# Performance work log

Hardware: AMD Instinct MI355X
Metric: run time of the kernel (lower is better)

Reference implementation:

```python
import jax, jax.numpy as jnp
import numpy as np

INPUT_DIM, HIDDEN, NUM_CLASSES = 16, 128, 24
B, T = 4096, 1024  # raw I/Q frame (B, 2, T); seq_len = 2*T/INPUT_DIM = 128


def setup_inputs() -> dict:
    key = jax.random.key(0)
    ks = jax.random.split(key, 12)
    s = 1.0 / np.sqrt(HIDDEN)  # torch default uniform bound ~ use scaled normal
    def w(k, shape, scale):
        return jax.random.normal(k, shape, jnp.float32) * scale
    return {
        "x": jax.random.normal(ks[0], (B, 2, T), jnp.float32),
        "w_ih1": w(ks[1], (3 * HIDDEN, INPUT_DIM), s),
        "w_hh1": w(ks[2], (3 * HIDDEN, HIDDEN), s),
        "b_ih1": w(ks[3], (3 * HIDDEN,), s),
        "b_hh1": w(ks[4], (3 * HIDDEN,), s),
        "w_ih2": w(ks[5], (3 * HIDDEN, HIDDEN), s),
        "w_hh2": w(ks[6], (3 * HIDDEN, HIDDEN), s),
        "b_ih2": w(ks[7], (3 * HIDDEN,), s),
        "b_hh2": w(ks[8], (3 * HIDDEN,), s),
        "fc_w": w(ks[9], (NUM_CLASSES, HIDDEN), s),
        "fc_b": w(ks[10], (NUM_CLASSES,), s),
    }


def _gru_layer(x, w_ih, w_hh, b_ih, b_hh, return_seq=True):
    # x: (B, L, D). PyTorch GRU gate order: r, z, n.
    Bb = x.shape[0]
    H = w_hh.shape[1]
    xp = jnp.einsum('bld,gd->blg', x, w_ih) + b_ih  # (B, L, 3H) precomputed input proj

    def step(h, xt):
        gh = h @ w_hh.T + b_hh  # (B, 3H)
        ir, iz, inn = jnp.split(xt, 3, axis=-1)
        hr, hz, hn = jnp.split(gh, 3, axis=-1)
        r = jax.nn.sigmoid(ir + hr)
        z = jax.nn.sigmoid(iz + hz)
        n = jnp.tanh(inn + r * hn)
        h_new = (1.0 - z) * n + z * h
        return h_new, (h_new if return_seq else 0.0)

    h0 = jnp.zeros((Bb, H), x.dtype)
    h_last, ys = jax.lax.scan(step, h0, jnp.swapaxes(xp, 0, 1))
    if return_seq:
        return jnp.swapaxes(ys, 0, 1)
    return h_last


def reference(x, w_ih1, w_hh1, b_ih1, b_hh1, w_ih2, w_hh2, b_ih2, b_hh2, fc_w, fc_b):
    Bb = x.shape[0]
    # (B,2,T) -> (B,2,L,8) -> (B,L,2,8) -> (B,L,16)
    h = x.reshape(Bb, 2, -1, INPUT_DIM // 2)
    h = jnp.swapaxes(h, 1, 2).reshape(Bb, -1, INPUT_DIM)
    seq1 = _gru_layer(h, w_ih1, w_hh1, b_ih1, b_hh1, return_seq=True)
    last = _gru_layer(seq1, w_ih2, w_hh2, b_ih2, b_hh2, return_seq=False)
    return last @ fc_w.T + fc_b
```

## Files before the change

### kernel.cpp

```cpp
#include <hip/hip_runtime.h>


typedef _Float16 half_t;
typedef _Float16 half8 __attribute__((ext_vector_type(8)));
typedef _Float16 half4v __attribute__((ext_vector_type(4)));
typedef float f32x4 __attribute__((ext_vector_type(4)));

#define BB 16
#define HS 136
#define XS 520

static __device__ __forceinline__ f32x4 mfma16(half8 a, half8 b, f32x4 c) {
  return __builtin_amdgcn_mfma_f32_16x16x32_f16(a, b, c, 0, 0, 0);
}

static __device__ __forceinline__ void pin(half8& v) {
  f32x4 t = __builtin_bit_cast(f32x4, v);
  asm volatile("" : "+v"(t));
  v = __builtin_bit_cast(half8, t);
}

static __device__ __forceinline__ half8 zero8() {
  half8 v;
#pragma unroll
  for (int i = 0; i < 8; ++i) v[i] = (half_t)0.f;
  return v;
}

static __device__ __forceinline__ half8 ldw8(const float* __restrict__ p) {
  float4 a = *(const float4*)p;
  float4 b = *(const float4*)(p + 4);
  half8 r;
  r[0] = (half_t)a.x; r[1] = (half_t)a.y; r[2] = (half_t)a.z; r[3] = (half_t)a.w;
  r[4] = (half_t)b.x; r[5] = (half_t)b.y; r[6] = (half_t)b.z; r[7] = (half_t)b.w;
  return r;
}

static __device__ __forceinline__ float sigm(float v) {
  return __builtin_amdgcn_rcpf(1.f + __expf(-v));
}
static __device__ __forceinline__ float tanh_fast(float v) {
  float e = __expf(2.f * v);
  return 1.f - 2.f * __builtin_amdgcn_rcpf(1.f + e);
}

__global__ __launch_bounds__(512, 2) void gru_fused(
    const float* __restrict__ x,
    const float* __restrict__ wih1, const float* __restrict__ whh1,
    const float* __restrict__ bih1, const float* __restrict__ bhh1,
    const float* __restrict__ wih2, const float* __restrict__ whh2,
    const float* __restrict__ bih2, const float* __restrict__ bhh2,
    const float* __restrict__ fcw, const float* __restrict__ fcb,
    float* __restrict__ out)
{
  __shared__ __align__(16) half_t xl[BB][XS];
  __shared__ __align__(16) half_t h1b[2][BB][HS];
  __shared__ __align__(16) half_t h2b[2][BB][HS];
  __shared__ float h2f[BB][129];

  const int tid = threadIdx.x;
  const int lane = tid & 63;
  const int wv = tid >> 6;
  const int q = lane >> 4;
  const int c = lane & 15;
  const int jc = wv * 16 + c;
  const int s0 = blockIdx.x * BB;

  for (int i = tid; i < 2 * BB * HS; i += 512) {
    ((half_t*)h1b)[i] = (half_t)0.f;
    ((half_t*)h2b)[i] = (half_t)0.f;
  }

  const float b1r  = bih1[jc]       + bhh1[jc];
  const float b1z  = bih1[128 + jc] + bhh1[128 + jc];
  const float b1in = bih1[256 + jc];
  const float b1hn = bhh1[256 + jc];
  const float b2r  = bih2[jc]       + bhh2[jc];
  const float b2z  = bih2[128 + jc] + bhh2[128 + jc];
  const float b2in = bih2[256 + jc];
  const float b2hn = bhh2[256 + jc];

  half8 wi1r, wi1z, wi1n;
  if (q < 2) {
    wi1r = ldw8(wih1 + (0 * 128 + jc) * 16 + q * 8);
    wi1z = ldw8(wih1 + (1 * 128 + jc) * 16 + q * 8);
    wi1n = ldw8(wih1 + (2 * 128 + jc) * 16 + q * 8);
  } else {
    wi1r = zero8(); wi1z = zero8(); wi1n = zero8();
  }
  pin(wi1r); pin(wi1z); pin(wi1n);

  half8 wh1r[4], wh1z[4], wh1n[4], wi2r[4], wi2z[4], wi2n[4], wh2r[4], wh2z[4], wh2n[4];
#pragma unroll
  for (int kk = 0; kk < 4; ++kk) {
    const int ko = kk * 32 + q * 8;
    wh1r[kk] = ldw8(whh1 + (0 * 128 + jc) * 128 + ko);
    wh1z[kk] = ldw8(whh1 + (1 * 128 + jc) * 128 + ko);
    wh1n[kk] = ldw8(whh1 + (2 * 128 + jc) * 128 + ko);
    wi2r[kk] = ldw8(wih2 + (0 * 128 + jc) * 128 + ko);
    wi2z[kk] = ldw8(wih2 + (1 * 128 + jc) * 128 + ko);
    wi2n[kk] = ldw8(wih2 + (2 * 128 + jc) * 128 + ko);
    wh2r[kk] = ldw8(whh2 + (0 * 128 + jc) * 128 + ko);
    wh2z[kk] = ldw8(whh2 + (1 * 128 + jc) * 128 + ko);
    wh2n[kk] = ldw8(whh2 + (2 * 128 + jc) * 128 + ko);
    pin(wh1r[kk]); pin(wh1z[kk]); pin(wh1n[kk]);
    pin(wi2r[kk]); pin(wi2z[kk]); pin(wi2n[kk]);
    pin(wh2r[kk]); pin(wh2z[kk]); pin(wh2n[kk]);
  }

  float h1p[4] = {0.f, 0.f, 0.f, 0.f};
  float h2p[4] = {0.f, 0.f, 0.f, 0.f};

  for (int tc = 0; tc < 4; ++tc) {
#pragma unroll
    for (int it = 0; it < 4; ++it) {
      int idx = tid + it * 512;
      int s = idx >> 7;
      int rem = idx & 127;
      int ch = rem >> 6;
      int i4 = rem & 63;
      const float4 v = *(const float4*)(x + (size_t)(s0 + s) * 2048 + ch * 1024 + tc * 256 + i4 * 4);
      half4v hv;
      hv[0] = (half_t)v.x; hv[1] = (half_t)v.y; hv[2] = (half_t)v.z; hv[3] = (half_t)v.w;
      *(half4v*)&xl[s][(i4 >> 1) * 16 + ch * 8 + (i4 & 1) * 4] = hv;
    }
    __syncthreads();

    for (int tt = 0; tt < 32; ++tt) {
      const int i = tc * 32 + tt;
      const int rb = i & 1;
      const int wb = rb ^ 1;

      f32x4 ar  = {b1r, b1r, b1r, b1r};
      f32x4 az  = {b1z, b1z, b1z, b1z};
      f32x4 ain = {b1in, b1in, b1in, b1in};
      f32x4 ahn = {b1hn, b1hn, b1hn, b1hn};
      f32x4 cr  = {b2r, b2r, b2r, b2r};
      f32x4 cz  = {b2z, b2z, b2z, b2z};
      f32x4 cin = {b2in, b2in, b2in, b2in};
      f32x4 chn = {b2hn, b2hn, b2hn, b2hn};

      {
        half8 ax = zero8();
        if (q < 2) ax = *(const half8*)&xl[c][tt * 16 + q * 8];
        ar  = mfma16(ax, wi1r, ar);
        az  = mfma16(ax, wi1z, az);
        ain = mfma16(ax, wi1n, ain);
      }
#pragma unroll
      for (int kk = 0; kk < 4; ++kk) {
        half8 ah = *(const half8*)&h1b[rb][c][kk * 32 + q * 8];
        half8 a2 = *(const half8*)&h2b[rb][c][kk * 32 + q * 8];
        ar  = mfma16(ah, wh1r[kk], ar);
        az  = mfma16(ah, wh1z[kk], az);
        ahn = mfma16(ah, wh1n[kk], ahn);
        cr  = mfma16(ah, wi2r[kk], cr);
        cz  = mfma16(ah, wi2z[kk], cz);
        cin = mfma16(ah, wi2n[kk], cin);
        cr  = mfma16(a2, wh2r[kk], cr);
        cz  = mfma16(a2, wh2z[kk], cz);
        chn = mfma16(a2, wh2n[kk], chn);
      }

#pragma unroll
      for (int r = 0; r < 4; ++r) {
        float rg = sigm(ar[r]);
        float zg = sigm(az[r]);
        float ng = tanh_fast(fmaf(rg, ahn[r], ain[r]));
        float hn = fmaf(zg, h1p[r] - ng, ng);
        h1p[r] = hn;
        h1b[wb][q * 4 + r][jc] = (half_t)hn;
      }
      if (i > 0) {
#pragma unroll
        for (int r = 0; r < 4; ++r) {
          float rg = sigm(cr[r]);
          float zg = sigm(cz[r]);
          float ng = tanh_fast(fmaf(rg, chn[r], cin[r]));
          float hn = fmaf(zg, h2p[r] - ng, ng);
          h2p[r] = hn;
          h2b[wb][q * 4 + r][jc] = (half_t)hn;
        }
      }
      __syncthreads();
    }
  }

  {
    f32x4 cr  = {b2r, b2r, b2r, b2r};
    f32x4 cz  = {b2z, b2z, b2z, b2z};
    f32x4 cin = {b2in, b2in, b2in, b2in};
    f32x4 chn = {b2hn, b2hn, b2hn, b2hn};
#pragma unroll
    for (int kk = 0; kk < 4; ++kk) {
      half8 a1 = *(const half8*)&h1b[0][c][kk * 32 + q * 8];
      half8 a2 = *(const half8*)&h2b[0][c][kk * 32 + q * 8];
      cr  = mfma16(a1, wi2r[kk], cr);
      cz  = mfma16(a1, wi2z[kk], cz);
      cin = mfma16(a1, wi2n[kk], cin);
      cr  = mfma16(a2, wh2r[kk], cr);
      cz  = mfma16(a2, wh2z[kk], cz);
      chn = mfma16(a2, wh2n[kk], chn);
    }
#pragma unroll
    for (int r = 0; r < 4; ++r) {
      float rg = sigm(cr[r]);
      float zg = sigm(cz[r]);
      float ng = tanh_fast(fmaf(rg, chn[r], cin[r]));
      h2p[r] = fmaf(zg, h2p[r] - ng, ng);
    }
  }

#pragma unroll
  for (int r = 0; r < 4; ++r) h2f[q * 4 + r][jc] = h2p[r];
  __syncthreads();
  if (tid < 384) {
    const int m = tid & 15;
    const int cls = tid >> 4;
    const float* w = fcw + cls * 128;
    float acc = fcb[cls];
#pragma unroll 8
    for (int j = 0; j < 128; ++j) acc = fmaf(h2f[m][j], w[j], acc);
    out[(size_t)(s0 + m) * 24 + cls] = acc;
  }
}

extern "C" void kernel_launch(void* const* d_in, const int* in_sizes, int n_in,
                              void* d_out, int out_size, void* d_ws, size_t ws_size,
                              hipStream_t stream) {
  (void)in_sizes; (void)n_in; (void)d_ws; (void)ws_size; (void)out_size;
  const float* x    = (const float*)d_in[0];
  const float* wih1 = (const float*)d_in[1];
  const float* whh1 = (const float*)d_in[2];
  const float* bih1 = (const float*)d_in[3];
  const float* bhh1 = (const float*)d_in[4];
  const float* wih2 = (const float*)d_in[5];
  const float* whh2 = (const float*)d_in[6];
  const float* bih2 = (const float*)d_in[7];
  const float* bhh2 = (const float*)d_in[8];
  const float* fcw  = (const float*)d_in[9];
  const float* fcb  = (const float*)d_in[10];
  float* outp = (float*)d_out;
  gru_fused<<<dim3(256), dim3(512), 0, stream>>>(
      x, wih1, whh1, bih1, bhh1, wih2, whh2, bih2, bhh2, fcw, fcb, outp);
}
```

Before: 277.3 us.

## Split fused two-layer GRU into separate layer kernels via fp16 workspace sequence

Replaces the single fused wavefront-style kernel with two kernels when the workspace is large enough. Layer 1 writes its hidden sequence in fp16 to global workspace in 8-step chunks, and layer 2 reads it back with register prefetch and double buffering. The aim is to cut per-kernel register pressure and shorten the per-step critical path. In exchange it adds about 128 MB of global write plus read traffic and serialises the two layers instead of overlapping them. The asm pin helpers are also removed.

```diff
diff --git a/kernel.cpp b/kernel.cpp
--- a/kernel.cpp
+++ b/kernel.cpp
@@ -12,12 +12,6 @@
 
 static __device__ __forceinline__ f32x4 mfma16(half8 a, half8 b, f32x4 c) {
   return __builtin_amdgcn_mfma_f32_16x16x32_f16(a, b, c, 0, 0, 0);
-}
-
-static __device__ __forceinline__ void pin(half8& v) {
-  f32x4 t = __builtin_bit_cast(f32x4, v);
-  asm volatile("" : "+v"(t));
-  v = __builtin_bit_cast(half8, t);
 }
 
 static __device__ __forceinline__ half8 zero8() {
@@ -42,6 +36,238 @@
 static __device__ __forceinline__ float tanh_fast(float v) {
   float e = __expf(2.f * v);
   return 1.f - 2.f * __builtin_amdgcn_rcpf(1.f + e);
+}
+
+__global__ __launch_bounds__(512, 2) void gru_l1(
+    const float* __restrict__ x,
+    const float* __restrict__ wih1, const float* __restrict__ whh1,
+    const float* __restrict__ bih1, const float* __restrict__ bhh1,
+    half_t* __restrict__ seq1)
+{
+  __shared__ __align__(16) half_t xl[BB][XS];
+  __shared__ __align__(16) half_t ost[8][BB][HS];
+
+  const int tid = threadIdx.x;
+  const int lane = tid & 63;
+  const int wv = tid >> 6;
+  const int q = lane >> 4;
+  const int c = lane & 15;
+  const int jc = wv * 16 + c;
+  const int s0 = blockIdx.x * BB;
+
+  for (int i = tid; i < 8 * BB * HS; i += 512) ((half_t*)ost)[i] = (half_t)0.f;
+
+  const float b1r  = bih1[jc]       + bhh1[jc];
+  const float b1z  = bih1[128 + jc] + bhh1[128 + jc];
+  const float b1in = bih1[256 + jc];
+  const float b1hn = bhh1[256 + jc];
+
+  half8 wi1r, wi1z, wi1n;
+  if (q < 2) {
+    wi1r = ldw8(wih1 + (0 * 128 + jc) * 16 + q * 8);
+    wi1z = ldw8(wih1 + (1 * 128 + jc) * 16 + q * 8);
+    wi1n = ldw8(wih1 + (2 * 128 + jc) * 16 + q * 8);
+  } else {
+    wi1r = zero8(); wi1z = zero8(); wi1n = zero8();
+  }
+  half8 wh1r[4], wh1z[4], wh1n[4];
+#pragma unroll
+  for (int kk = 0; kk < 4; ++kk) {
+    const int ko = kk * 32 + q * 8;
+    wh1r[kk] = ldw8(whh1 + (0 * 128 + jc) * 128 + ko);
+    wh1z[kk] = ldw8(whh1 + (1 * 128 + jc) * 128 + ko);
+    wh1n[kk] = ldw8(whh1 + (2 * 128 + jc) * 128 + ko);
+  }
+
+  float h1p[4] = {0.f, 0.f, 0.f, 0.f};
+
+  for (int g = 0; g < 16; ++g) {
+    if ((g & 3) == 0) {
+      const int tc = g >> 2;
+#pragma unroll
+      for (int it = 0; it < 4; ++it) {
+        int idx = tid + it * 512;
+        int s = idx >> 7;
+        int rem = idx & 127;
+        int ch = rem >> 6;
+        int i4 = rem & 63;
+        const float4 v = *(const float4*)(x + (size_t)(s0 + s) * 2048 + ch * 1024 + tc * 256 + i4 * 4);
+        half4v hv;
+        hv[0] = (half_t)v.x; hv[1] = (half_t)v.y; hv[2] = (half_t)v.z; hv[3] = (half_t)v.w;
+        *(half4v*)&xl[s][(i4 >> 1) * 16 + ch * 8 + (i4 & 1) * 4] = hv;
+      }
+      __syncthreads();
+    }
+
+    for (int tt = 0; tt < 8; ++tt) {
+      const int i = g * 8 + tt;
+      const int prev = (i + 7) & 7;
+
+      f32x4 ar  = {b1r, b1r, b1r, b1r};
+      f32x4 az  = {b1z, b1z, b1z, b1z};
+      f32x4 ain = {b1in, b1in, b1in, b1in};
+      f32x4 ahn = {b1hn, b1hn, b1hn, b1hn};
+      {
+        half8 ax = zero8();
+        if (q < 2) ax = *(const half8*)&xl[c][(i & 31) * 16 + q * 8];
+        ar  = mfma16(ax, wi1r, ar);
+        az  = mfma16(ax, wi1z, az);
+        ain = mfma16(ax, wi1n, ain);
+      }
+#pragma unroll
+      for (int kk = 0; kk < 4; ++kk) {
+        half8 ah = *(const half8*)&ost[prev][c][kk * 32 + q * 8];
+        ar  = mfma16(ah, wh1r[kk], ar);
+        az  = mfma16(ah, wh1z[kk], az);
+        ahn = mfma16(ah, wh1n[kk], ahn);
+      }
+#pragma unroll
+      for (int r = 0; r < 4; ++r) {
+        float rg = sigm(ar[r]);
+        float zg = sigm(az[r]);
+        float ng = tanh_fast(fmaf(rg, ahn[r], ain[r]));
+        float hn = fmaf(zg, h1p[r] - ng, ng);
+        h1p[r] = hn;
+        ost[tt][q * 4 + r][jc] = (half_t)hn;
+      }
+      __syncthreads();
+    }
+
+#pragma unroll
+    for (int p = 0; p < 4; ++p) {
+      int idx = tid + p * 512;
+      int col16 = idx & 15;
+      int row = (idx >> 4) & 15;
+      int st = idx >> 8;
+      f32x4 v = *(const f32x4*)&ost[st][row][col16 * 8];
+      size_t off = ((size_t)((s0 + row) * 128 + (g * 8 + st))) * 128 + col16 * 8;
+      *(f32x4*)(seq1 + off) = v;
+    }
+    __syncthreads();
+  }
+}
+
+__global__ __launch_bounds__(512, 2) void gru_l2(
+    const half_t* __restrict__ seq1,
+    const float* __restrict__ wih2, const float* __restrict__ whh2,
+    const float* __restrict__ bih2, const float* __restrict__ bhh2,
+    const float* __restrict__ fcw, const float* __restrict__ fcb,
+    float* __restrict__ out)
+{
+  __shared__ __align__(16) half_t sc[2][8][BB][HS];
+  __shared__ __align__(16) half_t h2b[2][BB][HS];
+  __shared__ float h2f[BB][129];
+
+  const int tid = threadIdx.x;
+  const int lane = tid & 63;
+  const int wv = tid >> 6;
+  const int q = lane >> 4;
+  const int c = lane & 15;
+  const int jc = wv * 16 + c;
+  const int s0 = blockIdx.x * BB;
+
+  for (int i = tid; i < BB * HS; i += 512) ((half_t*)h2b[0])[i] = (half_t)0.f;
+
+  const float b2r  = bih2[jc]       + bhh2[jc];
+  const float b2z  = bih2[128 + jc] + bhh2[128 + jc];
+  const float b2in = bih2[256 + jc];
+  const float b2hn = bhh2[256 + jc];
+
+  half8 wi2r[4], wi2z[4], wi2n[4], wh2r[4], wh2z[4], wh2n[4];
+#pragma unroll
+  for (int kk = 0; kk < 4; ++kk) {
+    const int ko = kk * 32 + q * 8;
+    wi2r[kk] = ldw8(wih2 + (0 * 128 + jc) * 128 + ko);
+    wi2z[kk] = ldw8(wih2 + (1 * 128 + jc) * 128 + ko);
+    wi2n[kk] = ldw8(wih2 + (2 * 128 + jc) * 128 + ko);
+    wh2r[kk] = ldw8(whh2 + (0 * 128 + jc) * 128 + ko);
+    wh2z[kk] = ldw8(whh2 + (1 * 128 + jc) * 128 + ko);
+    wh2n[kk] = ldw8(whh2 + (2 * 128 + jc) * 128 + ko);
+  }
+
+#pragma unroll
+  for (int p = 0; p < 4; ++p) {
+    int idx = tid + p * 512;
+    int col16 = idx & 15;
+    int row = (idx >> 4) & 15;
+    int st = idx >> 8;
+    size_t off = ((size_t)((s0 + row) * 128 + st)) * 128 + col16 * 8;
+    *(f32x4*)&sc[0][st][row][col16 * 8] = *(const f32x4*)(seq1 + off);
+  }
+  __syncthreads();
+
+  float h2p[4] = {0.f, 0.f, 0.f, 0.f};
+
+  for (int ch = 0; ch < 16; ++ch) {
+    f32x4 pf[4];
+    if (ch < 15) {
+#pragma unroll
+      for (int p = 0; p < 4; ++p) {
+        int idx = tid + p * 512;
+        int col16 = idx & 15;
+        int row = (idx >> 4) & 15;
+        int st = idx >> 8;
+        size_t off = ((size_t)((s0 + row) * 128 + ((ch + 1) * 8 + st))) * 128 + col16 * 8;
+        pf[p] = *(const f32x4*)(seq1 + off);
+      }
+    }
+    const int cb = ch & 1;
+
+    for (int tt = 0; tt < 8; ++tt) {
+      const int i = ch * 8 + tt;
+      const int rb = i & 1;
+      const int wb = rb ^ 1;
+
+      f32x4 cr  = {b2r, b2r, b2r, b2r};
+      f32x4 cz  = {b2z, b2z, b2z, b2z};
+      f32x4 cin = {b2in, b2in, b2in, b2in};
+      f32x4 chn = {b2hn, b2hn, b2hn, b2hn};
+#pragma unroll
+      for (int kk = 0; kk < 4; ++kk) {
+        half8 a1 = *(const half8*)&sc[cb][tt][c][kk * 32 + q * 8];
+        half8 a2 = *(const half8*)&h2b[rb][c][kk * 32 + q * 8];
+        cr  = mfma16(a1, wi2r[kk], cr);
+        cz  = mfma16(a1, wi2z[kk], cz);
+        cin = mfma16(a1, wi2n[kk], cin);
+        cr  = mfma16(a2, wh2r[kk], cr);
+        cz  = mfma16(a2, wh2z[kk], cz);
+        chn = mfma16(a2, wh2n[kk], chn);
+      }
+#pragma unroll
+      for (int r = 0; r < 4; ++r) {
+        float rg = sigm(cr[r]);
+        float zg = sigm(cz[r]);
+        float ng = tanh_fast(fmaf(rg, chn[r], cin[r]));
+        float hn = fmaf(zg, h2p[r] - ng, ng);
+        h2p[r] = hn;
+        h2b[wb][q * 4 + r][jc] = (half_t)hn;
+      }
+      if (tt == 7 && ch < 15) {
+#pragma unroll
+        for (int p = 0; p < 4; ++p) {
+          int idx = tid + p * 512;
+          int col16 = idx & 15;
+          int row = (idx >> 4) & 15;
+          int st = idx >> 8;
+          *(f32x4*)&sc[cb ^ 1][st][row][col16 * 8] = pf[p];
+        }
+      }
+      __syncthreads();
+    }
+  }
+
+#pragma unroll
+  for (int r = 0; r < 4; ++r) h2f[q * 4 + r][jc] = h2p[r];
+  __syncthreads();
+  if (tid < 384) {
+    const int m = tid & 15;
+    const int cls = tid >> 4;
+    const float* w = fcw + cls * 128;
+    float acc = fcb[cls];
+#pragma unroll 8
+    for (int j = 0; j < 128; ++j) acc = fmaf(h2f[m][j], w[j], acc);
+    out[(size_t)(s0 + m) * 24 + cls] = acc;
+  }
 }
 
 __global__ __launch_bounds__(512, 2) void gru_fused(
@@ -88,8 +314,6 @@
   } else {
     wi1r = zero8(); wi1z = zero8(); wi1n = zero8();
   }
-  pin(wi1r); pin(wi1z); pin(wi1n);
-
   half8 wh1r[4], wh1z[4], wh1n[4], wi2r[4], wi2z[4], wi2n[4], wh2r[4], wh2z[4], wh2n[4];
 #pragma unroll
   for (int kk = 0; kk < 4; ++kk) {
@@ -103,9 +327,6 @@
     wh2r[kk] = ldw8(whh2 + (0 * 128 + jc) * 128 + ko);
     wh2z[kk] = ldw8(whh2 + (1 * 128 + jc) * 128 + ko);
     wh2n[kk] = ldw8(whh2 + (2 * 128 + jc) * 128 + ko);
-    pin(wh1r[kk]); pin(wh1z[kk]); pin(wh1n[kk]);
-    pin(wi2r[kk]); pin(wi2z[kk]); pin(wi2n[kk]);
-    pin(wh2r[kk]); pin(wh2z[kk]); pin(wh2n[kk]);
   }
 
   float h1p[4] = {0.f, 0.f, 0.f, 0.f};
@@ -228,7 +449,7 @@
 extern "C" void kernel_launch(void* const* d_in, const int* in_sizes, int n_in,
                               void* d_out, int out_size, void* d_ws, size_t ws_size,
                               hipStream_t stream) {
-  (void)in_sizes; (void)n_in; (void)d_ws; (void)ws_size; (void)out_size;
+  (void)in_sizes; (void)n_in; (void)out_size;
   const float* x    = (const float*)d_in[0];
   const float* wih1 = (const float*)d_in[1];
   const float* whh1 = (const float*)d_in[2];
@@ -241,6 +462,14 @@
   const float* fcw  = (const float*)d_in[9];
   const float* fcb  = (const float*)d_in[10];
   float* outp = (float*)d_out;
-  gru_fused<<<dim3(256), dim3(512), 0, stream>>>(
-      x, wih1, whh1, bih1, bhh1, wih2, whh2, bih2, bhh2, fcw, fcb, outp);
-}
+
+  const size_t seq_bytes = (size_t)4096 * 128 * 128 * sizeof(half_t);
+  if (ws_size >= seq_bytes) {
+    half_t* seq1 = (half_t*)d_ws;
+    gru_l1<<<dim3(256), dim3(512), 0, stream>>>(x, wih1, whh1, bih1, bhh1, seq1);
+    gru_l2<<<dim3(256), dim3(512), 0, stream>>>(seq1, wih2, whh2, bih2, bhh2, fcw, fcb, outp);
+  } else {
+    gru_fused<<<dim3(256), dim3(512), 0, stream>>>(
+        x, wih1, whh1, bih1, bhh1, wih2, whh2, bih2, bhh2, fcw, fcb, outp);
+  }
+}
```

Measured after the change: 295.9 us. 6.7% more time.

## Split fused GRU into per-layer kernels with producer/consumer warp specialization

Applied to the files above, without the earlier changes.

Replaces the single fused two-layer kernel with two kernels: layer 1 writes its fp16 hidden sequence to workspace, and layer 2 reads it back and applies the final linear layer. Each kernel uses 1024 threads. Eight producer waves compute the input projection one step ahead into double-buffered LDS, while eight consumer waves run only the recurrent matmul and gates. The recurrence critical path per step drops from nine MFMAs per k-slice to three. The cost is a round trip of about 128 MB of intermediate sequence through global memory, and the whole path depends on the workspace being large enough; otherwise it falls back to the fused kernel.

```diff
diff --git a/kernel.cpp b/kernel.cpp
--- a/kernel.cpp
+++ b/kernel.cpp
@@ -6,18 +6,11 @@
 typedef _Float16 half4v __attribute__((ext_vector_type(4)));
 typedef float f32x4 __attribute__((ext_vector_type(4)));
 
-#define BB 16
 #define HS 136
 #define XS 520
 
 static __device__ __forceinline__ f32x4 mfma16(half8 a, half8 b, f32x4 c) {
   return __builtin_amdgcn_mfma_f32_16x16x32_f16(a, b, c, 0, 0, 0);
-}
-
-static __device__ __forceinline__ void pin(half8& v) {
-  f32x4 t = __builtin_bit_cast(f32x4, v);
-  asm volatile("" : "+v"(t));
-  v = __builtin_bit_cast(half8, t);
 }
 
 static __device__ __forceinline__ half8 zero8() {
@@ -42,6 +35,258 @@
 static __device__ __forceinline__ float tanh_fast(float v) {
   float e = __expf(2.f * v);
   return 1.f - 2.f * __builtin_amdgcn_rcpf(1.f + e);
+}
+
+__global__ __launch_bounds__(1024, 4) void gru_l1(
+    const float* __restrict__ x,
+    const float* __restrict__ wih1, const float* __restrict__ whh1,
+    const float* __restrict__ bih1, const float* __restrict__ bhh1,
+    half_t* __restrict__ seq1)
+{
+  __shared__ __align__(16) half_t xl[2][16][XS];
+  __shared__ __align__(16) half_t ost[8][16][HS];
+  __shared__ __align__(16) f32x4 xpb[2][8][3][64];
+
+  const int tid = threadIdx.x;
+  const int lane = tid & 63;
+  const int wv = tid >> 6;
+  const int q = lane >> 4;
+  const int c = lane & 15;
+  const bool prod = (wv >= 8);
+  const int cw = prod ? (wv - 8) : wv;
+  const int jc = cw * 16 + c;
+  const int s0 = blockIdx.x * 16;
+
+  for (int i = tid; i < 8 * 16 * HS; i += 1024) ((half_t*)ost)[i] = (half_t)0.f;
+
+#pragma unroll
+  for (int p = 0; p < 2; ++p) {
+    int idx = tid + p * 1024;
+    int s = idx >> 7, rem = idx & 127, chn = rem >> 6, i4 = rem & 63;
+    const float4 v = *(const float4*)(x + (size_t)(s0 + s) * 2048 + chn * 1024 + i4 * 4);
+    half4v hv;
+    hv[0] = (half_t)v.x; hv[1] = (half_t)v.y; hv[2] = (half_t)v.z; hv[3] = (half_t)v.w;
+    *(half4v*)&xl[0][s][(i4 >> 1) * 16 + chn * 8 + (i4 & 1) * 4] = hv;
+  }
+
+  half8 w[3][4];
+  if (prod) {
+#pragma unroll
+    for (int g = 0; g < 3; ++g) {
+      if (q < 2) w[g][0] = ldw8(wih1 + (g * 128 + jc) * 16 + q * 8);
+      else       w[g][0] = zero8();
+    }
+  } else {
+#pragma unroll
+    for (int g = 0; g < 3; ++g)
+#pragma unroll
+      for (int kk = 0; kk < 4; ++kk)
+        w[g][kk] = ldw8(whh1 + (g * 128 + jc) * 128 + kk * 32 + q * 8);
+  }
+  const float* bb = prod ? bih1 : bhh1;
+  const float b0 = bb[jc], b1 = bb[128 + jc], b2 = bb[256 + jc];
+
+  float h1p[4] = {0.f, 0.f, 0.f, 0.f};
+  __syncthreads();
+
+  if (prod) {
+    half8 ax = zero8();
+    if (q < 2) ax = *(const half8*)&xl[0][c][0 * 16 + q * 8];
+    f32x4 ir = {b0, b0, b0, b0}, iz = {b1, b1, b1, b1}, in_ = {b2, b2, b2, b2};
+    ir  = mfma16(ax, w[0][0], ir);
+    iz  = mfma16(ax, w[1][0], iz);
+    in_ = mfma16(ax, w[2][0], in_);
+    xpb[0][cw][0][lane] = ir; xpb[0][cw][1][lane] = iz; xpb[0][cw][2][lane] = in_;
+  }
+  __syncthreads();
+
+  for (int i = 0; i < 128; ++i) {
+    if ((i & 7) == 0 && i > 0) {
+      const int g8 = (i >> 3) - 1;
+#pragma unroll
+      for (int p = 0; p < 2; ++p) {
+        int idx = tid + p * 1024;
+        int col16 = idx & 15, row = (idx >> 4) & 15, st = idx >> 8;
+        f32x4 v = *(const f32x4*)&ost[st][row][col16 * 8];
+        *(f32x4*)(seq1 + ((size_t)((s0 + row) * 128 + g8 * 8 + st)) * 128 + col16 * 8) = v;
+      }
+      __syncthreads();
+    }
+
+    if (!prod) {
+      const int rd = (i + 7) & 7;
+      half8 f0 = *(const half8*)&ost[rd][c][0 * 32 + q * 8];
+      half8 f1 = *(const half8*)&ost[rd][c][1 * 32 + q * 8];
+      half8 f2 = *(const half8*)&ost[rd][c][2 * 32 + q * 8];
+      half8 f3 = *(const half8*)&ost[rd][c][3 * 32 + q * 8];
+      f32x4 xr = xpb[i & 1][cw][0][lane];
+      f32x4 xz = xpb[i & 1][cw][1][lane];
+      f32x4 xn = xpb[i & 1][cw][2][lane];
+      f32x4 hr = {b0, b0, b0, b0}, hz = {b1, b1, b1, b1}, hn = {b2, b2, b2, b2};
+      hr = mfma16(f0, w[0][0], hr); hz = mfma16(f0, w[1][0], hz); hn = mfma16(f0, w[2][0], hn);
+      hr = mfma16(f1, w[0][1], hr); hz = mfma16(f1, w[1][1], hz); hn = mfma16(f1, w[2][1], hn);
+      hr = mfma16(f2, w[0][2], hr); hz = mfma16(f2, w[1][2], hz); hn = mfma16(f2, w[2][2], hn);
+      hr = mfma16(f3, w[0][3], hr); hz = mfma16(f3, w[1][3], hz); hn = mfma16(f3, w[2][3], hn);
+#pragma unroll
+      for (int r = 0; r < 4; ++r) {
+        float rg = sigm(xr[r] + hr[r]);
+        float zg = sigm(xz[r] + hz[r]);
+        float ng = tanh_fast(fmaf(rg, hn[r], xn[r]));
+        float hne = fmaf(zg, h1p[r] - ng, ng);
+        h1p[r] = hne;
+        ost[i & 7][q * 4 + r][jc] = (half_t)hne;
+      }
+    } else {
+      if ((i & 7) == 0) {
+        int nc = (i >> 5) + 1;
+        if (nc < 4) {
+          int p = (i >> 3) & 3;
+          int idx = (wv - 8) * 64 + lane + p * 512;
+          int s = idx >> 7, rem = idx & 127, chn = rem >> 6, i4 = rem & 63;
+          const float4 v = *(const float4*)(x + (size_t)(s0 + s) * 2048 + chn * 1024 + nc * 256 + i4 * 4);
+          half4v hv;
+          hv[0] = (half_t)v.x; hv[1] = (half_t)v.y; hv[2] = (half_t)v.z; hv[3] = (half_t)v.w;
+          *(half4v*)&xl[nc & 1][s][(i4 >> 1) * 16 + chn * 8 + (i4 & 1) * 4] = hv;
+        }
+      }
+      if (i < 127) {
+        const int t1 = i + 1;
+        half8 ax = zero8();
+        if (q < 2) ax = *(const half8*)&xl[(t1 >> 5) & 1][c][(t1 & 31) * 16 + q * 8];
+        f32x4 ir = {b0, b0, b0, b0}, iz = {b1, b1, b1, b1}, in_ = {b2, b2, b2, b2};
+        ir  = mfma16(ax, w[0][0], ir);
+        iz  = mfma16(ax, w[1][0], iz);
+        in_ = mfma16(ax, w[2][0], in_);
+        xpb[t1 & 1][cw][0][lane] = ir;
+        xpb[t1 & 1][cw][1][lane] = iz;
+        xpb[t1 & 1][cw][2][lane] = in_;
+      }
+    }
+    __syncthreads();
+  }
+
+#pragma unroll
+  for (int p = 0; p < 2; ++p) {
+    int idx = tid + p * 1024;
+    int col16 = idx & 15, row = (idx >> 4) & 15, st = idx >> 8;
+    f32x4 v = *(const f32x4*)&ost[st][row][col16 * 8];
+    *(f32x4*)(seq1 + ((size_t)((s0 + row) * 128 + 15 * 8 + st)) * 128 + col16 * 8) = v;
+  }
+}
+
+__global__ __launch_bounds__(1024, 4) void gru_l2(
+    const half_t* __restrict__ seq1,
+    const float* __restrict__ wih2, const float* __restrict__ whh2,
+    const float* __restrict__ bih2, const float* __restrict__ bhh2,
+    const float* __restrict__ fcw, const float* __restrict__ fcb,
+    float* __restrict__ out)
+{
+  __shared__ __align__(16) half_t h2b[2][16][HS];
+  __shared__ __align__(16) f32x4 xpb[2][8][3][64];
+  __shared__ float h2f[16][132];
+
+  const int tid = threadIdx.x;
+  const int lane = tid & 63;
+  const int wv = tid >> 6;
+  const int q = lane >> 4;
+  const int c = lane & 15;
+  const bool prod = (wv >= 8);
+  const int cw = prod ? (wv - 8) : wv;
+  const int jc = cw * 16 + c;
+  const int s0 = blockIdx.x * 16;
+
+  for (int i = tid; i < 2 * 16 * HS; i += 1024) ((half_t*)h2b)[i] = (half_t)0.f;
+
+  const float* wbase = prod ? wih2 : whh2;
+  half8 w[3][4];
+#pragma unroll
+  for (int g = 0; g < 3; ++g)
+#pragma unroll
+    for (int kk = 0; kk < 4; ++kk)
+      w[g][kk] = ldw8(wbase + (g * 128 + jc) * 128 + kk * 32 + q * 8);
+  const float* bb = prod ? bih2 : bhh2;
+  const float b0 = bb[jc], b1 = bb[128 + jc], b2 = bb[256 + jc];
+
+  float h2p[4] = {0.f, 0.f, 0.f, 0.f};
+  f32x4 buf[2][4];
+
+  if (prod) {
+#pragma unroll
+    for (int kk = 0; kk < 4; ++kk)
+      buf[0][kk] = *(const f32x4*)(seq1 + ((size_t)(s0 + c) * 128 + 0) * 128 + kk * 32 + q * 8);
+    f32x4 ir = {b0, b0, b0, b0}, iz = {b1, b1, b1, b1}, in_ = {b2, b2, b2, b2};
+#pragma unroll
+    for (int kk = 0; kk < 4; ++kk) {
+      half8 a = __builtin_bit_cast(half8, buf[0][kk]);
+      ir  = mfma16(a, w[0][kk], ir);
+      iz  = mfma16(a, w[1][kk], iz);
+      in_ = mfma16(a, w[2][kk], in_);
+    }
+    xpb[0][cw][0][lane] = ir; xpb[0][cw][1][lane] = iz; xpb[0][cw][2][lane] = in_;
+#pragma unroll
+    for (int kk = 0; kk < 4; ++kk)
+      buf[1][kk] = *(const f32x4*)(seq1 + ((size_t)(s0 + c) * 128 + 1) * 128 + kk * 32 + q * 8);
+  }
+  __syncthreads();
+
+  for (int i = 0; i < 128; ++i) {
+    if (!prod) {
+      const int rs = (i + 1) & 1;
+      half8 f0 = *(const half8*)&h2b[rs][c][0 * 32 + q * 8];
+      half8 f1 = *(const half8*)&h2b[rs][c][1 * 32 + q * 8];
+      half8 f2 = *(const half8*)&h2b[rs][c][2 * 32 + q * 8];
+      half8 f3 = *(const half8*)&h2b[rs][c][3 * 32 + q * 8];
+      f32x4 xr = xpb[i & 1][cw][0][lane];
+      f32x4 xz = xpb[i & 1][cw][1][lane];
+      f32x4 xn = xpb[i & 1][cw][2][lane];
+      f32x4 hr = {b0, b0, b0, b0}, hz = {b1, b1, b1, b1}, hn = {b2, b2, b2, b2};
+      hr = mfma16(f0, w[0][0], hr); hz = mfma16(f0, w[1][0], hz); hn = mfma16(f0, w[2][0], hn);
+      hr = mfma16(f1, w[0][1], hr); hz = mfma16(f1, w[1][1], hz); hn = mfma16(f1, w[2][1], hn);
+      hr = mfma16(f2, w[0][2], hr); hz = mfma16(f2, w[1][2], hz); hn = mfma16(f2, w[2][2], hn);
+      hr = mfma16(f3, w[0][3], hr); hz = mfma16(f3, w[1][3], hz); hn = mfma16(f3, w[2][3], hn);
+#pragma unroll
+      for (int r = 0; r < 4; ++r) {
+        float rg = sigm(xr[r] + hr[r]);
+        float zg = sigm(xz[r] + hz[r]);
+        float ng = tanh_fast(fmaf(rg, hn[r], xn[r]));
+        float hne = fmaf(zg, h2p[r] - ng, ng);
+        h2p[r] = hne;
+        h2b[i & 1][q * 4 + r][jc] = (half_t)hne;
+      }
+    } else if (i < 127) {
+      const int bi = (i + 1) & 1;
+      if (i + 2 < 128) {
+#pragma unroll
+        for (int kk = 0; kk < 4; ++kk)
+          buf[bi ^ 1][kk] = *(const f32x4*)(seq1 + ((size_t)(s0 + c) * 128 + (i + 2)) * 128 + kk * 32 + q * 8);
+      }
+      f32x4 ir = {b0, b0, b0, b0}, iz = {b1, b1, b1, b1}, in_ = {b2, b2, b2, b2};
+#pragma unroll
+      for (int kk = 0; kk < 4; ++kk) {
+        half8 a = __builtin_bit_cast(half8, buf[bi][kk]);
+        ir  = mfma16(a, w[0][kk], ir);
+        iz  = mfma16(a, w[1][kk], iz);
+        in_ = mfma16(a, w[2][kk], in_);
+      }
+      xpb[bi][cw][0][lane] = ir; xpb[bi][cw][1][lane] = iz; xpb[bi][cw][2][lane] = in_;
+    }
+    __syncthreads();
+  }
+
+  if (!prod) {
+#pragma unroll
+    for (int r = 0; r < 4; ++r) h2f[q * 4 + r][jc] = h2p[r];
+  }
+  __syncthreads();
+  if (tid < 384) {
+    const int m = tid & 15;
+    const int cls = tid >> 4;
+    const float* fw = fcw + cls * 128;
+    float acc = fcb[cls];
+#pragma unroll 8
+    for (int j = 0; j < 128; ++j) acc = fmaf(h2f[m][j], fw[j], acc);
+    out[(size_t)(s0 + m) * 24 + cls] = acc;
+  }
 }
 
 __global__ __launch_bounds__(512, 2) void gru_fused(
@@ -53,10 +298,10 @@
     const float* __restrict__ fcw, const float* __restrict__ fcb,
     float* __restrict__ out)
 {
-  __shared__ __align__(16) half_t xl[BB][XS];
-  __shared__ __align__(16) half_t h1b[2][BB][HS];
-  __shared__ __align__(16) half_t h2b[2][BB][HS];
-  __shared__ float h2f[BB][129];
+  __shared__ __align__(16) half_t xl[16][XS];
+  __shared__ __align__(16) half_t h1b[2][16][HS];
+  __shared__ __align__(16) half_t h2b[2][16][HS];
+  __shared__ float h2f[16][129];
 
   const int tid = threadIdx.x;
   const int lane = tid & 63;
@@ -64,9 +309,9 @@
   const int q = lane >> 4;
   const int c = lane & 15;
   const int jc = wv * 16 + c;
-  const int s0 = blockIdx.x * BB;
-
-  for (int i = tid; i < 2 * BB * HS; i += 512) {
+  const int s0 = blockIdx.x * 16;
+
+  for (int i = tid; i < 2 * 16 * HS; i += 512) {
     ((half_t*)h1b)[i] = (half_t)0.f;
     ((half_t*)h2b)[i] = (half_t)0.f;
   }
@@ -88,8 +333,6 @@
   } else {
     wi1r = zero8(); wi1z = zero8(); wi1n = zero8();
   }
-  pin(wi1r); pin(wi1z); pin(wi1n);
-
   half8 wh1r[4], wh1z[4], wh1n[4], wi2r[4], wi2z[4], wi2n[4], wh2r[4], wh2z[4], wh2n[4];
 #pragma unroll
   for (int kk = 0; kk < 4; ++kk) {
@@ -103,9 +346,6 @@
     wh2r[kk] = ldw8(whh2 + (0 * 128 + jc) * 128 + ko);
     wh2z[kk] = ldw8(whh2 + (1 * 128 + jc) * 128 + ko);
     wh2n[kk] = ldw8(whh2 + (2 * 128 + jc) * 128 + ko);
-    pin(wh1r[kk]); pin(wh1z[kk]); pin(wh1n[kk]);
-    pin(wi2r[kk]); pin(wi2z[kk]); pin(wi2n[kk]);
-    pin(wh2r[kk]); pin(wh2z[kk]); pin(wh2n[kk]);
   }
 
   float h1p[4] = {0.f, 0.f, 0.f, 0.f};
@@ -117,12 +357,12 @@
       int idx = tid + it * 512;
       int s = idx >> 7;
       int rem = idx & 127;
-      int ch = rem >> 6;
+      int chn = rem >> 6;
       int i4 = rem & 63;
-      const float4 v = *(const float4*)(x + (size_t)(s0 + s) * 2048 + ch * 1024 + tc * 256 + i4 * 4);
+      const float4 v = *(const float4*)(x + (size_t)(s0 + s) * 2048 + chn * 1024 + tc * 256 + i4 * 4);
       half4v hv;
       hv[0] = (half_t)v.x; hv[1] = (half_t)v.y; hv[2] = (half_t)v.z; hv[3] = (half_t)v.w;
-      *(half4v*)&xl[s][(i4 >> 1) * 16 + ch * 8 + (i4 & 1) * 4] = hv;
+      *(half4v*)&xl[s][(i4 >> 1) * 16 + chn * 8 + (i4 & 1) * 4] = hv;
     }
     __syncthreads();
 
@@ -217,10 +457,10 @@
   if (tid < 384) {
     const int m = tid & 15;
     const int cls = tid >> 4;
-    const float* w = fcw + cls * 128;
+    const float* fw = fcw + cls * 128;
     float acc = fcb[cls];
 #pragma unroll 8
-    for (int j = 0; j < 128; ++j) acc = fmaf(h2f[m][j], w[j], acc);
+    for (int j = 0; j < 128; ++j) acc = fmaf(h2f[m][j], fw[j], acc);
     out[(size_t)(s0 + m) * 24 + cls] = acc;
   }
 }
@@ -228,7 +468,7 @@
 extern "C" void kernel_launch(void* const* d_in, const int* in_sizes, int n_in,
                               void* d_out, int out_size, void* d_ws, size_t ws_size,
                               hipStream_t stream) {
-  (void)in_sizes; (void)n_in; (void)d_ws; (void)ws_size; (void)out_size;
+  (void)in_sizes; (void)n_in; (void)out_size;
   const float* x    = (const float*)d_in[0];
   const float* wih1 = (const float*)d_in[1];
   const float* whh1 = (const float*)d_in[2];
@@ -241,6 +481,14 @@
   const float* fcw  = (const float*)d_in[9];
   const float* fcb  = (const float*)d_in[10];
   float* outp = (float*)d_out;
-  gru_fused<<<dim3(256), dim3(512), 0, stream>>>(
-      x, wih1, whh1, bih1, bhh1, wih2, whh2, bih2, bhh2, fcw, fcb, outp);
-}
+
+  const size_t seq_bytes = (size_t)4096 * 128 * 128 * sizeof(half_t);
+  if (ws_size >= seq_bytes) {
+    half_t* seq1 = (half_t*)d_ws;
+    gru_l1<<<dim3(256), dim3(1024), 0, stream>>>(x, wih1, whh1, bih1, bhh1, seq1);
+    gru_l2<<<dim3(256), dim3(1024), 0, stream>>>(seq1, wih2, whh2, bih2, bhh2, fcw, fcb, outp);
+  } else {
+    gru_fused<<<dim3(256), dim3(512), 0, stream>>>(
+        x, wih1, whh1, bih1, bhh1, wih2, whh2, bih2, bhh2, fcw, fcb, outp);
+  }
+}
```

Result: slower. 492.4 us (+77.5%).
